# Performance work log

Measured on AMD Instinct MI355X. Metric: run time of the kernel, lower is better.

## Reference

```python
import jax, jax.numpy as jnp
import numpy as np

N, H, CIN, C, G = 50000, 16, 256, 256, 8
CPG = C // G          # 32 channels per group
CR = C // 4           # delta MLP hidden (delta_reduction=4)

def _lrelu(x):
    return jax.nn.leaky_relu(x, 0.1)

def setup_inputs() -> dict:
    key = jax.random.key(0)
    ks = jax.random.split(key, 16)
    def lin(k, fin, fout):
        return jax.random.normal(k, (fin, fout), jnp.float32) / np.sqrt(fin)
    return {
        'q_pts': jax.random.normal(ks[0], (N, 3), jnp.float32),
        's_pts': jax.random.normal(ks[1], (N, 3), jnp.float32),
        's_feats': jax.random.normal(ks[2], (N, CIN), jnp.float32),
        'neighb_inds': jax.random.randint(ks[3], (N, H), 0, N, jnp.int64),
        'Wq': lin(ks[4], CIN, C), 'bq': jnp.zeros((C,), jnp.float32),
        'Wk': lin(ks[5], CIN, C), 'bk': jnp.zeros((C,), jnp.float32),
        'Wv': lin(ks[6], CIN, C), 'bv': jnp.zeros((C,), jnp.float32),
        'Wd1': lin(ks[7], 3, CR), 'bd1': jnp.zeros((CR,), jnp.float32),
        'Wd2': lin(ks[8], CR, C), 'bd2': jnp.zeros((C,), jnp.float32),
        'Wa1': lin(ks[9], C, CPG), 'ba1': jnp.zeros((CPG,), jnp.float32),
        'Wa2': lin(ks[10], CPG, CPG), 'ba2': jnp.zeros((CPG,), jnp.float32),
    }

def reference(q_pts, s_pts, s_feats, neighb_inds,
              Wq, bq, Wk, bk, Wv, bv,
              Wd1, bd1, Wd2, bd2, Wa1, ba1, Wa2, ba2):
    # q/k/v projections  (N, C)
    v = s_feats @ Wv + bv
    k = s_feats @ Wk + bk
    q = s_feats @ Wq + bq
    # gather neighbor features (all indices < N, shadow mask is a no-op)
    nv = v[neighb_inds]                 # (N, H, C)
    nk = k[neighb_inds]                 # (N, H, C)
    # relative positions (torch.no_grad in source)
    rel = s_pts[neighb_inds] - q_pts[:, None, :]   # (N, H, 3)
    # delta MLP: 3 -> C/4 -> C (UnaryBlock + Linear, norm='none')
    geom = _lrelu(rel @ Wd1 + bd1) @ Wd2 + bd2     # (N, H, C)
    # geom_mode='sub': v-branch and qk-branch both subtract geom encodings
    nv = nv - geom
    # source always enters strided branch (s_pts padded before the check);
    # stride_mode='nearest' -> q feature of the first neighbor
    qf = q[neighb_inds[:, 0]]                      # (N, C)
    qk = qf[:, None, :] - nk - geom                # (N, H, C)
    # alpha MLP: NormBlock(id) + act, Linear C->CpG + act, Linear CpG->CpG
    a = _lrelu(qk)
    a = _lrelu(a @ Wa1 + ba1)
    a = a @ Wa2 + ba2                              # (N, H, CpG)
    attn = jax.nn.softmax(a, axis=1)               # softmax over neighbors
    # grouped weighted aggregation: C split as (CpG, G), attn broadcast over G
    out = (nv.reshape(N, H, CPG, G) * attn[..., None]).sum(axis=1)
    return out.reshape(N, C)
```

## Files before the change

kernel.cpp:

```cpp
#include <hip/hip_runtime.h>
#include <cstdint>
#include <cstddef>

#define N_PTS 50000
#define H 16
#define CIN 256
#define C 256
#define CPG 32
#define CR 64

typedef short bf16x8 __attribute__((ext_vector_type(8)));
typedef float f32x4 __attribute__((ext_vector_type(4)));

__device__ __forceinline__ unsigned short f2bf(float f) {
    unsigned int u = __float_as_uint(f);
    u += 0x7fff + ((u >> 16) & 1);
    return (unsigned short)(u >> 16);
}
__device__ __forceinline__ float bf2f(unsigned short s) {
    return __uint_as_float(((unsigned int)s) << 16);
}

__global__ __launch_bounds__(256) void convert_feats(
    const float* __restrict__ in, unsigned short* __restrict__ outp)
{
    size_t i = ((size_t)blockIdx.x * 256 + threadIdx.x) * 8;
    float4 f0 = *(const float4*)&in[i];
    float4 f1 = *(const float4*)&in[i + 4];
    unsigned short t[8] = {f2bf(f0.x), f2bf(f0.y), f2bf(f0.z), f2bf(f0.w),
                           f2bf(f1.x), f2bf(f1.y), f2bf(f1.z), f2bf(f1.w)};
    *(bf16x8*)&outp[i] = *(bf16x8*)t;
}

__global__ __launch_bounds__(256) void prep_frags(
    const float* __restrict__ Wd2, const float* __restrict__ Wa1,
    const float* __restrict__ Wa2, unsigned short* __restrict__ dst)
{
    int t = blockIdx.x * 256 + threadIdx.x;
    if (t >= 3200) return;
    const float* W; int Nc, NT, loc, base;
    if (t < 2048)      { W = Wd2; Nc = 256; NT = 16; loc = t;        base = 0; }
    else if (t < 3072) { W = Wa1; Nc = 32;  NT = 2;  loc = t - 2048; base = 16384; }
    else               { W = Wa2; Nc = 32;  NT = 2;  loc = t - 3072; base = 24576; }
    int f = loc >> 6, lane = loc & 63;
    int kt = f / NT, nt = f - kt * NT;
    int colc = nt * 16 + (lane & 15);
    int row0 = kt * 32 + ((lane >> 4) << 3);
    unsigned short tmp[8];
    #pragma unroll
    for (int j = 0; j < 8; ++j) tmp[j] = f2bf(W[(size_t)(row0 + j) * Nc + colc]);
    *(bf16x8*)&dst[(size_t)(base + loc * 8)] = *(bf16x8*)tmp;
}

__global__ __launch_bounds__(256) void prep_gemm_frags(
    const float* __restrict__ Wq, const float* __restrict__ Wk,
    const float* __restrict__ Wv, unsigned short* __restrict__ dst)
{
    int t = blockIdx.x * 256 + threadIdx.x;
    int lane = t & 63;
    int f = t >> 6;
    int ntg = f % 48;
    const float* W = ntg < 16 ? Wq : (ntg < 32 ? Wk : Wv);
    int colc = (ntg & 15) * 16 + (lane & 15);
    int row0 = (f / 48) * 32 + ((lane >> 4) << 3);
    unsigned short tmp[8];
    #pragma unroll
    for (int j = 0; j < 8; ++j) tmp[j] = f2bf(W[(size_t)(row0 + j) * 256 + colc]);
    *(bf16x8*)&dst[(size_t)t * 8] = *(bf16x8*)tmp;
}

__global__ __launch_bounds__(256) void qkv_gemm_mfma(
    const unsigned short* __restrict__ A,
    const unsigned short* __restrict__ wfrags,
    const float* __restrict__ bq, const float* __restrict__ bk,
    const float* __restrict__ bv, unsigned short* __restrict__ out)
{
    __shared__ unsigned short s_a[128 * 40];
    const int tid = threadIdx.x;
    const int lane = tid & 63, wave = tid >> 6;
    const int quad = lane >> 4, col16 = lane & 15;
    const int bx = blockIdx.x, by = blockIdx.y;

    f32x4 acc[2][8] = {};
    const int mrow = tid >> 1, half = tid & 1;
    const int gm = by * 128 + mrow;

    for (int kt = 0; kt < 8; ++kt) {
        bf16x8 a0 = {0,0,0,0,0,0,0,0}, a1 = a0;
        if (gm < N_PTS) {
            const unsigned short* src = &A[(size_t)gm * 256 + kt * 32 + half * 16];
            a0 = *(const bf16x8*)src;
            a1 = *(const bf16x8*)(src + 8);
        }
        __syncthreads();
        *(bf16x8*)&s_a[mrow * 40 + half * 16]     = a0;
        *(bf16x8*)&s_a[mrow * 40 + half * 16 + 8] = a1;
        __syncthreads();
        bf16x8 af0 = *(bf16x8*)&s_a[(wave * 32 + col16) * 40 + quad * 8];
        bf16x8 af1 = *(bf16x8*)&s_a[(wave * 32 + 16 + col16) * 40 + quad * 8];
        #pragma unroll
        for (int nt = 0; nt < 8; ++nt) {
            bf16x8 bf = *(const bf16x8*)&wfrags[(((size_t)kt * 48 + bx * 8 + nt) * 64 + lane) * 8];
            acc[0][nt] = __builtin_amdgcn_mfma_f32_16x16x32_bf16(af0, bf, acc[0][nt], 0, 0, 0);
            acc[1][nt] = __builtin_amdgcn_mfma_f32_16x16x32_bf16(af1, bf, acc[1][nt], 0, 0, 0);
        }
    }

    const int mode = bx >> 1;
    const float* bias = mode == 0 ? bq : (mode == 1 ? bk : bv);
    #pragma unroll
    for (int nt = 0; nt < 8; ++nt) {
        int cIn = (bx & 1) * 128 + nt * 16 + col16;
        float bb = bias[cIn];
        int pos = mode == 0 ? cIn : (256 + 2 * cIn + (mode == 2 ? 1 : 0));
        #pragma unroll
        for (int mt = 0; mt < 2; ++mt) {
            #pragma unroll
            for (int r = 0; r < 4; ++r) {
                int row = by * 128 + wave * 32 + mt * 16 + quad * 4 + r;
                if (row < N_PTS)
                    out[(size_t)row * 768 + pos] = f2bf(acc[mt][nt][r] + bb);
            }
        }
    }
}

#define D1S 72
#define GS 260
#define QKS 264
#define A1S 40
#define A2S 33

__global__ __launch_bounds__(256) void attn_mfma(
    const unsigned short* __restrict__ qkv,
    const float* __restrict__ q_pts, const float* __restrict__ s_pts,
    const int* __restrict__ nbr,
    const float* __restrict__ Wd1, const float* __restrict__ bd1,
    const float* __restrict__ bd2,
    const unsigned short* __restrict__ frags,
    const float* __restrict__ ba1, const float* __restrict__ ba2,
    float* __restrict__ out)
{
    __shared__ unsigned short s_d1[H * D1S];
    __shared__ float          s_geom[H * GS];
    __shared__ unsigned short s_qk[H * QKS];
    __shared__ unsigned short s_a1[H * A1S];
    __shared__ float          s_a2[H * A2S];
    __shared__ float          s_rel[4][H][3];
    __shared__ int            s_idx[4][H];

    const int tid = threadIdx.x;
    const int lane = tid & 63, wave = tid >> 6;
    const int quad = lane >> 4, col = lane & 15;
    const int n0 = blockIdx.x * 4;
    const int c = tid;

    if (tid < 64) {
        int pp = tid >> 4, hh = tid & 15;
        int idx = nbr[(size_t)(n0 + pp) * H + hh];
        s_idx[pp][hh] = idx;
        #pragma unroll
        for (int x = 0; x < 3; ++x)
            s_rel[pp][hh][x] = s_pts[(size_t)idx * 3 + x] - q_pts[(size_t)(n0 + pp) * 3 + x];
    }

    const float w1x = Wd1[lane], w1y = Wd1[64 + lane], w1z = Wd1[128 + lane];
    const float b1 = bd1[lane];
    const float b2 = bd2[c];
    bf16x8 wd2f[2][4];
    #pragma unroll
    for (int t = 0; t < 4; ++t) {
        wd2f[0][t] = *(const bf16x8*)&frags[((size_t)((0 * 16 + wave * 4 + t) * 64 + lane)) * 8];
        wd2f[1][t] = *(const bf16x8*)&frags[((size_t)((1 * 16 + wave * 4 + t) * 64 + lane)) * 8];
    }
    bf16x8 wa1f[8];
    bf16x8 wa2f = {0,0,0,0,0,0,0,0};
    if (wave < 2) {
        #pragma unroll
        for (int kt = 0; kt < 8; ++kt)
            wa1f[kt] = *(const bf16x8*)&frags[16384 + ((size_t)((kt * 2 + wave) * 64 + lane)) * 8];
        wa2f = *(const bf16x8*)&frags[24576 + ((size_t)(wave * 64 + lane)) * 8];
    }
    __syncthreads();

    for (int p = 0; p < 4; ++p) {
        const int n = n0 + p;

        #pragma unroll
        for (int pass = 0; pass < 4; ++pass) {
            int h = pass * 4 + wave;
            float v = b1 + s_rel[p][h][0] * w1x + s_rel[p][h][1] * w1y + s_rel[p][h][2] * w1z;
            s_d1[h * D1S + lane] = f2bf(fmaxf(v, 0.1f * v));
        }
        __syncthreads();

        {
            bf16x8 ga = *(bf16x8*)&s_d1[col * D1S + quad * 8];
            bf16x8 gb = *(bf16x8*)&s_d1[col * D1S + 32 + quad * 8];
            #pragma unroll
            for (int t = 0; t < 4; ++t) {
                f32x4 acc = {0.f, 0.f, 0.f, 0.f};
                acc = __builtin_amdgcn_mfma_f32_16x16x32_bf16(ga, wd2f[0][t], acc, 0, 0, 0);
                acc = __builtin_amdgcn_mfma_f32_16x16x32_bf16(gb, wd2f[1][t], acc, 0, 0, 0);
                int nt = wave * 4 + t;
                #pragma unroll
                for (int rr = 0; rr < 4; ++rr)
                    s_geom[(quad * 4 + rr) * GS + nt * 16 + col] = acc[rr];
            }
        }
        __syncthreads();

        float qf = bf2f(qkv[(size_t)s_idx[p][0] * 768 + c]);
        float vg[H];
        #pragma unroll
        for (int h = 0; h < H; ++h) {
            int idx = s_idx[p][h];
            unsigned int u = *(const unsigned int*)&qkv[(size_t)idx * 768 + 256 + 2 * c];
            float nk = __uint_as_float(u << 16);
            float nv = __uint_as_float(u & 0xffff0000u);
            float g = s_geom[h * GS + c] + b2;
            vg[h] = nv - g;
            float tq = qf - nk - g;
            s_qk[h * QKS + c] = f2bf(fmaxf(tq, 0.1f * tq));
        }
        __syncthreads();

        if (wave < 2) {
            f32x4 acc = {0.f, 0.f, 0.f, 0.f};
            #pragma unroll
            for (int kt = 0; kt < 8; ++kt) {
                bf16x8 a = *(bf16x8*)&s_qk[col * QKS + kt * 32 + quad * 8];
                acc = __builtin_amdgcn_mfma_f32_16x16x32_bf16(a, wa1f[kt], acc, 0, 0, 0);
            }
            int j = wave * 16 + col;
            float bb = ba1[j];
            #pragma unroll
            for (int rr = 0; rr < 4; ++rr) {
                float v = acc[rr] + bb;
                s_a1[(quad * 4 + rr) * A1S + j] = f2bf(fmaxf(v, 0.1f * v));
            }
        }
        __syncthreads();

        if (wave < 2) {
            bf16x8 aa = *(bf16x8*)&s_a1[col * A1S + quad * 8];
            f32x4 acc = {0.f, 0.f, 0.f, 0.f};
            acc = __builtin_amdgcn_mfma_f32_16x16x32_bf16(aa, wa2f, acc, 0, 0, 0);
            int j = wave * 16 + col;
            float bb = ba2[j];
            #pragma unroll
            for (int rr = 0; rr < 4; ++rr)
                s_a2[(quad * 4 + rr) * A2S + j] = acc[rr] + bb;
        }
        __syncthreads();

        if (wave == 0) {
            int j = lane & 31, hb = (lane >> 5) * 8;
            float vals[8];
            float mx = -1e30f;
            #pragma unroll
            for (int i = 0; i < 8; ++i) {
                vals[i] = s_a2[(hb + i) * A2S + j];
                mx = fmaxf(mx, vals[i]);
            }
            mx = fmaxf(mx, __shfl_xor(mx, 32));
            float sum = 0.f;
            #pragma unroll
            for (int i = 0; i < 8; ++i) { vals[i] = __expf(vals[i] - mx); sum += vals[i]; }
            sum += __shfl_xor(sum, 32);
            float inv = 1.f / sum;
            #pragma unroll
            for (int i = 0; i < 8; ++i) s_a2[(hb + i) * A2S + j] = vals[i] * inv;
        }
        __syncthreads();

        float o = 0.f;
        const int aj = c >> 3;
        #pragma unroll
        for (int h = 0; h < H; ++h) o += vg[h] * s_a2[h * A2S + aj];
        out[(size_t)n * C + c] = o;
    }
}


extern "C" void kernel_launch(void* const* d_in, const int* in_sizes, int n_in,
                              void* d_out, int out_size, void* d_ws, size_t ws_size,
                              hipStream_t stream) {
    const float* q_pts   = (const float*)d_in[0];
    const float* s_pts   = (const float*)d_in[1];
    const float* s_feats = (const float*)d_in[2];
    const int*   nbr     = (const int*)d_in[3];
    const float* Wq  = (const float*)d_in[4];
    const float* bq  = (const float*)d_in[5];
    const float* Wk  = (const float*)d_in[6];
    const float* bk  = (const float*)d_in[7];
    const float* Wv  = (const float*)d_in[8];
    const float* bv  = (const float*)d_in[9];
    const float* Wd1 = (const float*)d_in[10];
    const float* bd1 = (const float*)d_in[11];
    const float* Wd2 = (const float*)d_in[12];
    const float* bd2 = (const float*)d_in[13];
    const float* Wa1 = (const float*)d_in[14];
    const float* ba1 = (const float*)d_in[15];
    const float* Wa2 = (const float*)d_in[16];
    const float* ba2 = (const float*)d_in[17];

    float* out = (float*)d_out;
    char* ws = (char*)d_ws;
    unsigned short* A_bf16    = (unsigned short*)(ws);
    unsigned short* qkvb      = (unsigned short*)(ws + 25600000);
    unsigned short* attnFrags = (unsigned short*)(ws + 102400000);
    unsigned short* gemmFrags = (unsigned short*)(ws + 102451200);

    convert_feats<<<6250, 256, 0, stream>>>(s_feats, A_bf16);
    prep_frags<<<13, 256, 0, stream>>>(Wd2, Wa1, Wa2, attnFrags);
    prep_gemm_frags<<<96, 256, 0, stream>>>(Wq, Wk, Wv, gemmFrags);

    dim3 g1(6, (N_PTS + 127) / 128);
    qkv_gemm_mfma<<<g1, 256, 0, stream>>>(A_bf16, gemmFrags, bq, bk, bv, qkvb);

    attn_mfma<<<(N_PTS / 4), 256, 0, stream>>>(qkvb, q_pts, s_pts, nbr,
                                               Wd1, bd1, bd2, attnFrags,
                                               ba1, ba2, out);
}
```

Before: 426.9 us.

## Merge prep kernels and keep geom per wave to drop a barrier

Merges the three preprocessing kernels into one launch. In the attention kernel each wave writes its own geom tile to a private shared buffer, so one block-wide barrier per point goes away. The 16 neighbour k/v gathers are issued before the geom MFMA so their latency overlaps it, and the kernel requests 3 blocks per SM via launch bounds. Holding all 16 gathered values in registers raises register pressure, and the launch bound may force spills.

```diff
diff --git a/kernel.cpp b/kernel.cpp
--- a/kernel.cpp
+++ b/kernel.cpp
@@ -21,52 +21,52 @@
     return __uint_as_float(((unsigned int)s) << 16);
 }
 
-__global__ __launch_bounds__(256) void convert_feats(
-    const float* __restrict__ in, unsigned short* __restrict__ outp)
+__global__ __launch_bounds__(256) void prep_all(
+    const float* __restrict__ feats,
+    const float* __restrict__ Wq, const float* __restrict__ Wk,
+    const float* __restrict__ Wv,
+    const float* __restrict__ Wd2, const float* __restrict__ Wa1,
+    const float* __restrict__ Wa2,
+    unsigned short* __restrict__ A_bf16,
+    unsigned short* __restrict__ gemmFrags,
+    unsigned short* __restrict__ attnFrags)
 {
-    size_t i = ((size_t)blockIdx.x * 256 + threadIdx.x) * 8;
-    float4 f0 = *(const float4*)&in[i];
-    float4 f1 = *(const float4*)&in[i + 4];
-    unsigned short t[8] = {f2bf(f0.x), f2bf(f0.y), f2bf(f0.z), f2bf(f0.w),
-                           f2bf(f1.x), f2bf(f1.y), f2bf(f1.z), f2bf(f1.w)};
-    *(bf16x8*)&outp[i] = *(bf16x8*)t;
-}
-
-__global__ __launch_bounds__(256) void prep_frags(
-    const float* __restrict__ Wd2, const float* __restrict__ Wa1,
-    const float* __restrict__ Wa2, unsigned short* __restrict__ dst)
-{
-    int t = blockIdx.x * 256 + threadIdx.x;
-    if (t >= 3200) return;
-    const float* W; int Nc, NT, loc, base;
-    if (t < 2048)      { W = Wd2; Nc = 256; NT = 16; loc = t;        base = 0; }
-    else if (t < 3072) { W = Wa1; Nc = 32;  NT = 2;  loc = t - 2048; base = 16384; }
-    else               { W = Wa2; Nc = 32;  NT = 2;  loc = t - 3072; base = 24576; }
-    int f = loc >> 6, lane = loc & 63;
-    int kt = f / NT, nt = f - kt * NT;
-    int colc = nt * 16 + (lane & 15);
-    int row0 = kt * 32 + ((lane >> 4) << 3);
-    unsigned short tmp[8];
-    #pragma unroll
-    for (int j = 0; j < 8; ++j) tmp[j] = f2bf(W[(size_t)(row0 + j) * Nc + colc]);
-    *(bf16x8*)&dst[(size_t)(base + loc * 8)] = *(bf16x8*)tmp;
-}
-
-__global__ __launch_bounds__(256) void prep_gemm_frags(
-    const float* __restrict__ Wq, const float* __restrict__ Wk,
-    const float* __restrict__ Wv, unsigned short* __restrict__ dst)
-{
-    int t = blockIdx.x * 256 + threadIdx.x;
-    int lane = t & 63;
-    int f = t >> 6;
-    int ntg = f % 48;
-    const float* W = ntg < 16 ? Wq : (ntg < 32 ? Wk : Wv);
-    int colc = (ntg & 15) * 16 + (lane & 15);
-    int row0 = (f / 48) * 32 + ((lane >> 4) << 3);
-    unsigned short tmp[8];
-    #pragma unroll
-    for (int j = 0; j < 8; ++j) tmp[j] = f2bf(W[(size_t)(row0 + j) * 256 + colc]);
-    *(bf16x8*)&dst[(size_t)t * 8] = *(bf16x8*)tmp;
+    int bid = blockIdx.x;
+    if (bid < 6250) {
+        size_t i = ((size_t)bid * 256 + threadIdx.x) * 8;
+        float4 f0 = *(const float4*)&feats[i];
+        float4 f1 = *(const float4*)&feats[i + 4];
+        unsigned short t[8] = {f2bf(f0.x), f2bf(f0.y), f2bf(f0.z), f2bf(f0.w),
+                               f2bf(f1.x), f2bf(f1.y), f2bf(f1.z), f2bf(f1.w)};
+        *(bf16x8*)&A_bf16[i] = *(bf16x8*)t;
+    } else if (bid < 6346) {
+        int t = (bid - 6250) * 256 + threadIdx.x;
+        int lane = t & 63;
+        int f = t >> 6;
+        int ntg = f % 48;
+        const float* W = ntg < 16 ? Wq : (ntg < 32 ? Wk : Wv);
+        int colc = (ntg & 15) * 16 + (lane & 15);
+        int row0 = (f / 48) * 32 + ((lane >> 4) << 3);
+        unsigned short tmp[8];
+        #pragma unroll
+        for (int j = 0; j < 8; ++j) tmp[j] = f2bf(W[(size_t)(row0 + j) * 256 + colc]);
+        *(bf16x8*)&gemmFrags[(size_t)t * 8] = *(bf16x8*)tmp;
+    } else {
+        int t = (bid - 6346) * 256 + threadIdx.x;
+        if (t >= 3200) return;
+        const float* W; int Nc, NT, loc, base;
+        if (t < 2048)      { W = Wd2; Nc = 256; NT = 16; loc = t;        base = 0; }
+        else if (t < 3072) { W = Wa1; Nc = 32;  NT = 2;  loc = t - 2048; base = 16384; }
+        else               { W = Wa2; Nc = 32;  NT = 2;  loc = t - 3072; base = 24576; }
+        int f = loc >> 6, lane = loc & 63;
+        int kt = f / NT, nt = f - kt * NT;
+        int colc = nt * 16 + (lane & 15);
+        int row0 = kt * 32 + ((lane >> 4) << 3);
+        unsigned short tmp[8];
+        #pragma unroll
+        for (int j = 0; j < 8; ++j) tmp[j] = f2bf(W[(size_t)(row0 + j) * Nc + colc]);
+        *(bf16x8*)&attnFrags[(size_t)(base + loc * 8)] = *(bf16x8*)tmp;
+    }
 }
 
 __global__ __launch_bounds__(256) void qkv_gemm_mfma(
@@ -126,12 +126,12 @@
 }
 
 #define D1S 72
-#define GS 260
+#define PGS 66
 #define QKS 264
 #define A1S 40
 #define A2S 33
 
-__global__ __launch_bounds__(256) void attn_mfma(
+__global__ __launch_bounds__(256, 3) void attn_mfma(
     const unsigned short* __restrict__ qkv,
     const float* __restrict__ q_pts, const float* __restrict__ s_pts,
     const int* __restrict__ nbr,
@@ -142,7 +142,7 @@
     float* __restrict__ out)
 {
     __shared__ unsigned short s_d1[H * D1S];
-    __shared__ float          s_geom[H * GS];
+    __shared__ float          s_pg[4 * H * PGS];
     __shared__ unsigned short s_qk[H * QKS];
     __shared__ unsigned short s_a1[H * A1S];
     __shared__ float          s_a2[H * A2S];
@@ -183,6 +183,8 @@
     }
     __syncthreads();
 
+    float* pg = &s_pg[wave * (H * PGS)];
+
     for (int p = 0; p < 4; ++p) {
         const int n = n0 + p;
 
@@ -194,6 +196,12 @@
         }
         __syncthreads();
 
+        unsigned int u[H];
+        #pragma unroll
+        for (int h = 0; h < H; ++h)
+            u[h] = *(const unsigned int*)&qkv[(size_t)s_idx[p][h] * 768 + 256 + 2 * c];
+        float qf = bf2f(qkv[(size_t)s_idx[p][0] * 768 + c]);
+
         {
             bf16x8 ga = *(bf16x8*)&s_d1[col * D1S + quad * 8];
             bf16x8 gb = *(bf16x8*)&s_d1[col * D1S + 32 + quad * 8];
@@ -202,23 +210,18 @@
                 f32x4 acc = {0.f, 0.f, 0.f, 0.f};
                 acc = __builtin_amdgcn_mfma_f32_16x16x32_bf16(ga, wd2f[0][t], acc, 0, 0, 0);
                 acc = __builtin_amdgcn_mfma_f32_16x16x32_bf16(gb, wd2f[1][t], acc, 0, 0, 0);
-                int nt = wave * 4 + t;
                 #pragma unroll
                 for (int rr = 0; rr < 4; ++rr)
-                    s_geom[(quad * 4 + rr) * GS + nt * 16 + col] = acc[rr];
-            }
-        }
-        __syncthreads();
-
-        float qf = bf2f(qkv[(size_t)s_idx[p][0] * 768 + c]);
+                    pg[(quad * 4 + rr) * PGS + t * 16 + col] = acc[rr];
+            }
+        }
+
         float vg[H];
         #pragma unroll
         for (int h = 0; h < H; ++h) {
-            int idx = s_idx[p][h];
-            unsigned int u = *(const unsigned int*)&qkv[(size_t)idx * 768 + 256 + 2 * c];
-            float nk = __uint_as_float(u << 16);
-            float nv = __uint_as_float(u & 0xffff0000u);
-            float g = s_geom[h * GS + c] + b2;
+            float g = pg[h * PGS + lane] + b2;
+            float nk = __uint_as_float(u[h] << 16);
+            float nv = __uint_as_float(u[h] & 0xffff0000u);
             vg[h] = nv - g;
             float tq = qf - nk - g;
             s_qk[h * QKS + c] = f2bf(fmaxf(tq, 0.1f * tq));
@@ -312,9 +315,8 @@
     unsigned short* attnFrags = (unsigned short*)(ws + 102400000);
     unsigned short* gemmFrags = (unsigned short*)(ws + 102451200);
 
-    convert_feats<<<6250, 256, 0, stream>>>(s_feats, A_bf16);
-    prep_frags<<<13, 256, 0, stream>>>(Wd2, Wa1, Wa2, attnFrags);
-    prep_gemm_frags<<<96, 256, 0, stream>>>(Wq, Wk, Wv, gemmFrags);
+    prep_all<<<6359, 256, 0, stream>>>(s_feats, Wq, Wk, Wv, Wd2, Wa1, Wa2,
+                                       A_bf16, gemmFrags, attnFrags);
 
     dim3 g1(6, (N_PTS + 127) / 128);
     qkv_gemm_mfma<<<g1, 256, 0, stream>>>(A_bf16, gemmFrags, bq, bk, bv, qkvb);
```

New measurement: 404.1 us. 1.06x faster.
